# Kernel tuning notes

Hardware: AMD Instinct MI355X
Metric: run time of the kernel (lower is better)

Reference implementation:

```python
import jax, jax.numpy as jnp
import numpy as np

D_MODEL = 768
N_HEADS = 12
HEAD_DIM = D_MODEL // N_HEADS
D_FF = 4 * D_MODEL
EPS = 1e-5


def setup_inputs() -> dict:
    key = jax.random.key(0)
    ks = jax.random.split(key, 16)
    s = 0.02
    x = jax.random.normal(ks[0], (2, 2048, D_MODEL), dtype=jnp.float32)
    wq = jax.random.normal(ks[1], (D_MODEL, D_MODEL), dtype=jnp.float32) * s
    bq = jnp.zeros((D_MODEL,), jnp.float32)
    wk = jax.random.normal(ks[2], (D_MODEL, D_MODEL), dtype=jnp.float32) * s
    bk = jnp.zeros((D_MODEL,), jnp.float32)
    wv = jax.random.normal(ks[3], (D_MODEL, D_MODEL), dtype=jnp.float32) * s
    bv = jnp.zeros((D_MODEL,), jnp.float32)
    wo = jax.random.normal(ks[4], (D_MODEL, D_MODEL), dtype=jnp.float32) * s
    bo = jnp.zeros((D_MODEL,), jnp.float32)
    w1 = jax.random.normal(ks[5], (D_MODEL, D_FF), dtype=jnp.float32) * s
    b1 = jnp.zeros((D_FF,), jnp.float32)
    w2 = jax.random.normal(ks[6], (D_FF, D_MODEL), dtype=jnp.float32) * s
    b2 = jnp.zeros((D_MODEL,), jnp.float32)
    ln1_g = jnp.ones((D_MODEL,), jnp.float32)
    ln1_b = jnp.zeros((D_MODEL,), jnp.float32)
    ln2_g = jnp.ones((D_MODEL,), jnp.float32)
    ln2_b = jnp.zeros((D_MODEL,), jnp.float32)
    return dict(x=x, wq=wq, bq=bq, wk=wk, bk=bk, wv=wv, bv=bv, wo=wo, bo=bo,
                w1=w1, b1=b1, w2=w2, b2=b2,
                ln1_g=ln1_g, ln1_b=ln1_b, ln2_g=ln2_g, ln2_b=ln2_b)


def _layernorm(x, g, b):
    mu = jnp.mean(x, axis=-1, keepdims=True)
    var = jnp.mean(jnp.square(x - mu), axis=-1, keepdims=True)
    return (x - mu) * jax.lax.rsqrt(var + EPS) * g + b


def _attention(x, wq, bq, wk, bk, wv, bv, wo, bo):
    B, S, D = x.shape
    def split_heads(t):  # [B,S,D] -> [B,H,S,Hd]
        return t.reshape(B, S, N_HEADS, HEAD_DIM).transpose(0, 2, 1, 3)
    q = split_heads(x @ wq + bq)
    k = split_heads(x @ wk + bk)
    v = split_heads(x @ wv + bv)
    scores = jnp.einsum('bhqd,bhkd->bhqk', q, k) / np.sqrt(HEAD_DIM).astype(np.float32)
    causal = jnp.tril(jnp.ones((S, S), dtype=bool))
    scores = jnp.where(causal, scores, -jnp.inf)
    weights = jax.nn.softmax(scores, axis=-1)
    attn = jnp.einsum('bhqk,bhkd->bhqd', weights, v)
    attn = attn.transpose(0, 2, 1, 3).reshape(B, S, D)
    return attn @ wo + bo


def reference(x, wq, bq, wk, bk, wv, bv, wo, bo, w1, b1, w2, b2,
              ln1_g, ln1_b, ln2_g, ln2_b):
    x = x + _attention(_layernorm(x, ln1_g, ln1_b), wq, bq, wk, bk, wv, bv, wo, bo)
    h = _layernorm(x, ln2_g, ln2_b)
    ff = jax.nn.relu(h @ w1 + b1) @ w2 + b2
    return x + ff
```

## Files before the change

kernel.cpp:

```cpp
#include <hip/hip_runtime.h>
#include <stdint.h>

typedef __bf16 bf16;
typedef float f32x4 __attribute__((ext_vector_type(4)));
typedef bf16 bf16x8 __attribute__((ext_vector_type(8)));
typedef bf16 bf16x4 __attribute__((ext_vector_type(4)));

#define MFMA16(a, b, c) __builtin_amdgcn_mfma_f32_16x16x32_bf16((a), (b), (c), 0, 0, 0)

static __device__ __forceinline__ void load_lds16(const bf16* g, bf16* l) {
  __builtin_amdgcn_global_load_lds(
      (const __attribute__((address_space(1))) void*)g,
      (__attribute__((address_space(3))) void*)l, 16, 0, 0);
}

__global__ void __launch_bounds__(256) k_transpose(
    const float* s0, const float* s1, const float* s2, const float* s3,
    const float* s4, const float* s5,
    bf16* d0, bf16* d1, bf16* d2, bf16* d3, bf16* d4, bf16* d5) {
  int z = blockIdx.z;
  const float* src; bf16* dst; int R, C;
  switch (z) {
    case 0: src = s0; dst = d0; R = 768;  C = 768;  break;
    case 1: src = s1; dst = d1; R = 768;  C = 768;  break;
    case 2: src = s2; dst = d2; R = 768;  C = 768;  break;
    case 3: src = s3; dst = d3; R = 768;  C = 768;  break;
    case 4: src = s4; dst = d4; R = 768;  C = 3072; break;
    default: src = s5; dst = d5; R = 3072; C = 768; break;
  }
  int tcn = C >> 5;
  int nt = (R >> 5) * tcn;
  int t = blockIdx.x;
  if (t >= nt) return;
  int tr = t / tcn, tc = t % tcn;
  __shared__ float tile[32][33];
  int tx = threadIdx.x & 31, ty = threadIdx.x >> 5;
  for (int i = 0; i < 4; i++)
    tile[ty + i * 8][tx] = src[(size_t)(tr * 32 + ty + i * 8) * C + tc * 32 + tx];
  __syncthreads();
  for (int i = 0; i < 4; i++)
    dst[(size_t)(tc * 32 + ty + i * 8) * R + tr * 32 + tx] = (bf16)tile[tx][ty + i * 8];
}

__global__ void __launch_bounds__(256) k_layernorm(
    const float* __restrict__ in, const float* __restrict__ gam,
    const float* __restrict__ bet, bf16* __restrict__ out) {
  int row = blockIdx.x, tid = threadIdx.x;
  const float* rp = in + (size_t)row * 768;
  float v0 = rp[tid], v1 = rp[tid + 256], v2 = rp[tid + 512];
  float s = v0 + v1 + v2, sq = v0 * v0 + v1 * v1 + v2 * v2;
  for (int off = 1; off < 64; off <<= 1) {
    s += __shfl_xor(s, off, 64);
    sq += __shfl_xor(sq, off, 64);
  }
  __shared__ float ps[8];
  if ((tid & 63) == 0) { ps[tid >> 6] = s; ps[4 + (tid >> 6)] = sq; }
  __syncthreads();
  s = ps[0] + ps[1] + ps[2] + ps[3];
  sq = ps[4] + ps[5] + ps[6] + ps[7];
  float mu = s * (1.0f / 768.0f);
  float rstd = rsqrtf(sq * (1.0f / 768.0f) - mu * mu + 1e-5f);
  bf16* op = out + (size_t)row * 768;
  op[tid] = (bf16)((v0 - mu) * rstd * gam[tid] + bet[tid]);
  op[tid + 256] = (bf16)((v1 - mu) * rstd * gam[tid + 256] + bet[tid + 256]);
  op[tid + 512] = (bf16)((v2 - mu) * rstd * gam[tid + 512] + bet[tid + 512]);
}

__global__ void __launch_bounds__(256) k_ln2_reduce(
    const float* __restrict__ p0, const float* __restrict__ p1,
    const float* __restrict__ x, const float* __restrict__ bo,
    const float* __restrict__ gam, const float* __restrict__ bet,
    float* __restrict__ x1, bf16* __restrict__ h2) {
  int row = blockIdx.x, tid = threadIdx.x;
  size_t base = (size_t)row * 768;
  float v0 = p0[base + tid] + p1[base + tid] + x[base + tid] + bo[tid];
  float v1 = p0[base + tid + 256] + p1[base + tid + 256] + x[base + tid + 256] + bo[tid + 256];
  float v2 = p0[base + tid + 512] + p1[base + tid + 512] + x[base + tid + 512] + bo[tid + 512];
  x1[base + tid] = v0; x1[base + tid + 256] = v1; x1[base + tid + 512] = v2;
  float s = v0 + v1 + v2, sq = v0 * v0 + v1 * v1 + v2 * v2;
  for (int off = 1; off < 64; off <<= 1) {
    s += __shfl_xor(s, off, 64);
    sq += __shfl_xor(sq, off, 64);
  }
  __shared__ float ps[8];
  if ((tid & 63) == 0) { ps[tid >> 6] = s; ps[4 + (tid >> 6)] = sq; }
  __syncthreads();
  s = ps[0] + ps[1] + ps[2] + ps[3];
  sq = ps[4] + ps[5] + ps[6] + ps[7];
  float mu = s * (1.0f / 768.0f);
  float rstd = rsqrtf(sq * (1.0f / 768.0f) - mu * mu + 1e-5f);
  bf16* op = h2 + base;
  op[tid] = (bf16)((v0 - mu) * rstd * gam[tid] + bet[tid]);
  op[tid + 256] = (bf16)((v1 - mu) * rstd * gam[tid + 256] + bet[tid + 256]);
  op[tid + 512] = (bf16)((v2 - mu) * rstd * gam[tid + 512] + bet[tid + 512]);
}

__global__ void __launch_bounds__(256) k_ff2_reduce(
    const float* __restrict__ f0, const float* __restrict__ f1,
    const float* __restrict__ f2, const float* __restrict__ f3,
    const float* __restrict__ x1, const float* __restrict__ b2,
    float* __restrict__ out) {
  size_t i = ((size_t)blockIdx.x * 256 + threadIdx.x) * 4;
  int col = (int)(i % 768);
  f32x4 v = *(const f32x4*)(x1 + i);
  f32x4 b = *(const f32x4*)(b2 + col);
  f32x4 a0 = *(const f32x4*)(f0 + i), a1 = *(const f32x4*)(f1 + i);
  f32x4 a2 = *(const f32x4*)(f2 + i), a3 = *(const f32x4*)(f3 + i);
  *(f32x4*)(out + i) = v + b + a0 + a1 + a2 + a3;
}

template <int MT>
static __device__ __forceinline__ void gemm_core(
    const bf16* __restrict__ A, int lda, const bf16* __restrict__ Bt, int ldb,
    int Kc, int m0, int n0, bf16* As, bf16* Bs, f32x4 acc[MT][4]) {
  int tid = threadIdx.x, w = tid >> 6, lane = tid & 63, quad = lane >> 4, l15 = lane & 15;
  int wr = w >> 1, wc = w & 1;
  int srow = lane >> 2, sk = (lane & 3) * 8;
  for (int k0 = 0; k0 < Kc; k0 += 32) {
    __syncthreads();
    if (MT == 4) {
      for (int c = 0; c < 2; c++) {
        int seg = w * 2 + c;
        load_lds16(A + (size_t)(m0 + seg * 16 + srow) * lda + k0 + sk, As + seg * 512);
      }
    } else {
      load_lds16(A + (size_t)(m0 + w * 16 + srow) * lda + k0 + sk, As + w * 512);
    }
    for (int c = 0; c < 2; c++) {
      int seg = w * 2 + c;
      load_lds16(Bt + (size_t)(n0 + seg * 16 + srow) * ldb + k0 + sk, Bs + seg * 512);
    }
    __syncthreads();
    bf16x8 af[MT], bfr[4];
    for (int mi = 0; mi < MT; mi++)
      af[mi] = *(const bf16x8*)(As + (wr * (MT * 16) + mi * 16 + l15) * 32 + quad * 8);
    for (int ni = 0; ni < 4; ni++)
      bfr[ni] = *(const bf16x8*)(Bs + (wc * 64 + ni * 16 + l15) * 32 + quad * 8);
    for (int mi = 0; mi < MT; mi++)
      for (int ni = 0; ni < 4; ni++)
        acc[mi][ni] = MFMA16(af[mi], bfr[ni], acc[mi][ni]);
  }
}

template <int MT>
__global__ void __launch_bounds__(256) k_gemm(
    const bf16* __restrict__ A, const bf16* __restrict__ Bt,
    const float* __restrict__ bias, bf16* __restrict__ outp, int K_, int N_) {
  __shared__ __align__(16) bf16 As[MT * 32 * 32];
  __shared__ __align__(16) bf16 Bs[128 * 32];
  int m0 = blockIdx.y * (MT * 32), n0 = blockIdx.x * 128;
  f32x4 acc[MT][4] = {};
  gemm_core<MT>(A, K_, Bt, K_, K_, m0, n0, As, Bs, acc);
  int tid = threadIdx.x, w = tid >> 6, lane = tid & 63, quad = lane >> 4, l15 = lane & 15;
  int wr = w >> 1, wc = w & 1;
  float bv[4];
  for (int ni = 0; ni < 4; ni++) bv[ni] = bias[n0 + wc * 64 + ni * 16 + l15];
  for (int mi = 0; mi < MT; mi++) {
    int mb = m0 + wr * (MT * 16) + mi * 16 + quad * 4;
    for (int ni = 0; ni < 4; ni++) {
      int n = n0 + wc * 64 + ni * 16 + l15;
      for (int r = 0; r < 4; r++) {
        float val = acc[mi][ni][r] + bv[ni];
        outp[(size_t)(mb + r) * N_ + n] = (bf16)fmaxf(val, 0.0f);
      }
    }
  }
}

template <int MT>
__global__ void __launch_bounds__(256) k_gemm_split(
    const bf16* __restrict__ A, const bf16* __restrict__ Bt,
    float* __restrict__ f0, float* __restrict__ f1,
    float* __restrict__ f2, float* __restrict__ f3, int K_, int Kc, int N_) {
  __shared__ __align__(16) bf16 As[MT * 32 * 32];
  __shared__ __align__(16) bf16 Bs[128 * 32];
  int z = blockIdx.z;
  float* outp = (z == 0) ? f0 : (z == 1) ? f1 : (z == 2) ? f2 : f3;
  int m0 = blockIdx.y * (MT * 32), n0 = blockIdx.x * 128;
  f32x4 acc[MT][4] = {};
  gemm_core<MT>(A + (size_t)z * Kc, K_, Bt + (size_t)z * Kc, K_, Kc, m0, n0, As, Bs, acc);
  int tid = threadIdx.x, w = tid >> 6, lane = tid & 63, quad = lane >> 4, l15 = lane & 15;
  int wr = w >> 1, wc = w & 1;
  for (int mi = 0; mi < MT; mi++) {
    int mb = m0 + wr * (MT * 16) + mi * 16 + quad * 4;
    for (int ni = 0; ni < 4; ni++) {
      int n = n0 + wc * 64 + ni * 16 + l15;
      for (int r = 0; r < 4; r++)
        outp[(size_t)(mb + r) * N_ + n] = acc[mi][ni][r];
    }
  }
}

template <int MT>
__global__ void __launch_bounds__(256) k_gemm_qkv(
    const bf16* __restrict__ h1, const bf16* __restrict__ wqT,
    const bf16* __restrict__ wkT, const bf16* __restrict__ wvT,
    const float* __restrict__ bq, const float* __restrict__ bk,
    const float* __restrict__ bv, bf16* __restrict__ qb,
    bf16* __restrict__ kb, bf16* __restrict__ vtb) {
  __shared__ __align__(16) bf16 As[MT * 32 * 32];
  __shared__ __align__(16) bf16 Bs[128 * 32];
  int z = blockIdx.z;
  const bf16* Bt = (z == 0) ? wqT : (z == 1) ? wkT : wvT;
  const float* bias = (z == 0) ? bq : (z == 1) ? bk : bv;
  int m0 = blockIdx.y * (MT * 32), n0 = blockIdx.x * 128;
  f32x4 acc[MT][4] = {};
  gemm_core<MT>(h1, 768, Bt, 768, 768, m0, n0, As, Bs, acc);
  int tid = threadIdx.x, w = tid >> 6, lane = tid & 63, quad = lane >> 4, l15 = lane & 15;
  int wr = w >> 1, wc = w & 1;
  float bvv[4];
  for (int ni = 0; ni < 4; ni++) bvv[ni] = bias[n0 + wc * 64 + ni * 16 + l15];
  for (int mi = 0; mi < MT; mi++) {
    int mb = m0 + wr * (MT * 16) + mi * 16 + quad * 4;
    int b = mb >> 11, s0_ = mb & 2047;
    for (int ni = 0; ni < 4; ni++) {
      int n = n0 + wc * 64 + ni * 16 + l15;
      int h = n >> 6, hd = n & 63;
      if (z < 2) {
        bf16* outp = (z == 0) ? qb : kb;
        size_t base = (size_t)(b * 12 + h) * 2048 * 64;
        for (int r = 0; r < 4; r++)
          outp[base + (size_t)(s0_ + r) * 64 + hd] = (bf16)(acc[mi][ni][r] + bvv[ni]);
      } else {
        bf16x4 pk;
        for (int r = 0; r < 4; r++) pk[r] = (bf16)(acc[mi][ni][r] + bvv[ni]);
        *(bf16x4*)(vtb + (((size_t)(b * 12 + h) * 64 + hd) * 2048 + s0_)) = pk;
      }
    }
  }
}

__global__ void __launch_bounds__(256) k_attn(
    const bf16* __restrict__ qb, const bf16* __restrict__ kb,
    const bf16* __restrict__ vtb, bf16* __restrict__ out) {
  __shared__ __align__(16) bf16 Ks[128 * 64];
  __shared__ __align__(16) bf16 Vs[64 * 128];
  __shared__ __align__(16) bf16 Ps[4][16 * 128];
  int qt = 31 - (blockIdx.x / 24);
  int bh = blockIdx.x % 24;
  int q0 = qt * 64;
  int tid = threadIdx.x, w = tid >> 6, lane = tid & 63, quad = lane >> 4, l15 = lane & 15;
  const bf16* qbase = qb + (size_t)bh * 2048 * 64;
  const bf16* kbase = kb + (size_t)bh * 2048 * 64;
  const bf16* vbase = vtb + (size_t)bh * 64 * 2048;

  bf16x8 qf[2];
  for (int ds = 0; ds < 2; ds++)
    qf[ds] = *(const bf16x8*)(qbase + (size_t)(q0 + w * 16 + l15) * 64 + ds * 32 + quad * 8);

  f32x4 o[4] = {};
  f32x4 l_i = {};

  const float C2 = 0.18033688011112042f;
  int nkt = (qt >> 1) + 1;
  for (int kt = 0; kt < nkt; kt++) {
    int k0 = kt * 128;
    __syncthreads();
    {
      int rsub = lane >> 3, c8 = lane & 7;
      for (int c = 0; c < 4; c++) {
        int seg = c * 4 + w;
        int row = seg * 8 + rsub;
        load_lds16(kbase + (size_t)(k0 + row) * 64 + ((c8 ^ (row & 7)) * 8), Ks + seg * 512);
      }
      int rsub2 = lane >> 4, c16 = lane & 15;
      for (int c = 0; c < 4; c++) {
        int seg = c * 4 + w;
        int row = seg * 4 + rsub2;
        load_lds16(vbase + (size_t)row * 2048 + k0 + ((c16 ^ (row & 15)) * 8), Vs + seg * 512);
      }
    }
    __syncthreads();

    f32x4 sc[8] = {};
    for (int kj = 0; kj < 8; kj++) {
      int krow = kj * 16 + l15;
      for (int ds = 0; ds < 2; ds++) {
        bf16x8 kf = *(const bf16x8*)(Ks + krow * 64 + (((ds * 4 + quad) ^ (krow & 7)) * 8));
        sc[kj] = MFMA16(qf[ds], kf, sc[kj]);
      }
    }
    if (kt == nkt - 1) {
      int qg = q0 + w * 16 + quad * 4;
      for (int kj = 0; kj < 8; kj++) {
        int kg = k0 + kj * 16 + l15;
        for (int r = 0; r < 4; r++)
          if (kg > qg + r) sc[kj][r] = -3.0e38f;
      }
    }
    f32x4 lsum = {};
    for (int kj = 0; kj < 8; kj++)
      for (int r = 0; r < 4; r++) {
        float p = exp2f(sc[kj][r] * C2);
        sc[kj][r] = p;
        lsum[r] += p;
      }
    for (int off = 1; off < 16; off <<= 1)
      for (int r = 0; r < 4; r++) lsum[r] += __shfl_xor(lsum[r], off, 64);
    for (int r = 0; r < 4; r++) l_i[r] += lsum[r];
    for (int kj = 0; kj < 8; kj++) {
      int colb = kj * 16 + l15;
      int chb = colb >> 3, cin = colb & 7;
      for (int r = 0; r < 4; r++) {
        int prow = quad * 4 + r;
        Ps[w][prow * 128 + ((chb ^ prow) * 8) + cin] = (bf16)sc[kj][r];
      }
    }
    for (int ks = 0; ks < 4; ks++) {
      int prow = l15;
      bf16x8 pf = *(const bf16x8*)(&Ps[w][prow * 128 + (((ks * 4 + quad) ^ prow) * 8)]);
      for (int dj = 0; dj < 4; dj++) {
        int vrow = dj * 16 + l15;
        bf16x8 vf = *(const bf16x8*)(Vs + vrow * 128 + (((ks * 4 + quad) ^ (vrow & 15)) * 8));
        o[dj] = MFMA16(pf, vf, o[dj]);
      }
    }
  }
  int b = bh / 12, h = bh % 12;
  f32x4 rl;
  for (int r = 0; r < 4; r++) rl[r] = 1.0f / l_i[r];
  int srow = q0 + w * 16 + quad * 4;
  for (int dj = 0; dj < 4; dj++) {
    int d = h * 64 + dj * 16 + l15;
    for (int r = 0; r < 4; r++)
      out[(size_t)(b * 2048 + srow + r) * 768 + d] = (bf16)(o[dj][r] * rl[r]);
  }
}

extern "C" void kernel_launch(void* const* d_in, const int* in_sizes, int n_in,
                              void* d_out, int out_size, void* d_ws, size_t ws_size,
                              hipStream_t stream) {
  const float* x    = (const float*)d_in[0];
  const float* wq   = (const float*)d_in[1];
  const float* bq   = (const float*)d_in[2];
  const float* wk   = (const float*)d_in[3];
  const float* bk   = (const float*)d_in[4];
  const float* wv   = (const float*)d_in[5];
  const float* bv   = (const float*)d_in[6];
  const float* wo   = (const float*)d_in[7];
  const float* bo   = (const float*)d_in[8];
  const float* w1   = (const float*)d_in[9];
  const float* b1   = (const float*)d_in[10];
  const float* w2   = (const float*)d_in[11];
  const float* b2   = (const float*)d_in[12];
  const float* ln1g = (const float*)d_in[13];
  const float* ln1b = (const float*)d_in[14];
  const float* ln2g = (const float*)d_in[15];
  const float* ln2b = (const float*)d_in[16];

  char* p = (char*)d_ws;
  bf16* wqT = (bf16*)p; p += (size_t)768 * 768 * 2;
  bf16* wkT = (bf16*)p; p += (size_t)768 * 768 * 2;
  bf16* wvT = (bf16*)p; p += (size_t)768 * 768 * 2;
  bf16* woT = (bf16*)p; p += (size_t)768 * 768 * 2;
  bf16* w1T = (bf16*)p; p += (size_t)768 * 3072 * 2;
  bf16* w2T = (bf16*)p; p += (size_t)768 * 3072 * 2;
  bf16* h1   = (bf16*)p; p += (size_t)4096 * 768 * 2;
  bf16* qbuf = (bf16*)p; p += (size_t)4096 * 768 * 2;
  bf16* kbuf = (bf16*)p; p += (size_t)4096 * 768 * 2;
  bf16* vtb  = (bf16*)p; p += (size_t)4096 * 768 * 2;
  bf16* att  = (bf16*)p; p += (size_t)4096 * 768 * 2;
  float* x1  = (float*)p; p += (size_t)4096 * 768 * 4;
  bf16* h2   = (bf16*)p; p += (size_t)4096 * 768 * 2;
  bf16* ffm  = (bf16*)p; p += (size_t)4096 * 3072 * 2;
  float* p0  = (float*)p; p += (size_t)4096 * 768 * 4;
  float* p1  = (float*)p; p += (size_t)4096 * 768 * 4;
  float* f0 = (float*)h1;
  float* f1 = (float*)kbuf;
  float* f2 = p0;
  float* f3 = p1;

  k_transpose<<<dim3(2304, 1, 6), dim3(256), 0, stream>>>(
      wq, wk, wv, wo, w1, w2, wqT, wkT, wvT, woT, w1T, w2T);
  k_layernorm<<<dim3(4096), dim3(256), 0, stream>>>(x, ln1g, ln1b, h1);
  k_gemm_qkv<2><<<dim3(6, 64, 3), dim3(256), 0, stream>>>(
      h1, wqT, wkT, wvT, bq, bk, bv, qbuf, kbuf, vtb);
  k_attn<<<dim3(768), dim3(256), 0, stream>>>(qbuf, kbuf, vtb, att);
  k_gemm_split<2><<<dim3(6, 64, 2), dim3(256), 0, stream>>>(
      att, woT, p0, p1, p0, p1, 768, 384, 768);
  k_ln2_reduce<<<dim3(4096), dim3(256), 0, stream>>>(
      p0, p1, x, bo, ln2g, ln2b, x1, h2);
  k_gemm<2><<<dim3(24, 64), dim3(256), 0, stream>>>(
      h2, w1T, b1, ffm, 768, 3072);
  k_gemm_split<2><<<dim3(6, 64, 4), dim3(256), 0, stream>>>(
      ffm, w2T, f0, f1, f2, f3, 3072, 768, 768);
  k_ff2_reduce<<<dim3(3072), dim3(256), 0, stream>>>(
      f0, f1, f2, f3, x1, b2, (float*)d_out);
}
```

Baseline: 316.8 us.

## Replace split-K partial buffers with atomic accumulation and enlarge GEMM tiles

Split-K GEMMs now atomically add their partial sums straight into the residual buffers, which are pre-seeded with residual plus bias by the layernorm kernels. This removes the separate reduce kernels and the partial-buffer traffic. All GEMMs move to 128x128 tiles with a changed LDS load/read layout, so each block gets more reuse but the grids have fewer blocks. Float atomics make the summation order nondeterministic and add atomic traffic to global memory.

```diff
diff --git a/kernel.cpp b/kernel.cpp
--- a/kernel.cpp
+++ b/kernel.cpp
@@ -12,6 +12,10 @@
   __builtin_amdgcn_global_load_lds(
       (const __attribute__((address_space(1))) void*)g,
       (__attribute__((address_space(3))) void*)l, 16, 0, 0);
+}
+
+static __device__ __forceinline__ void atomAdd(float* p, float v) {
+  __hip_atomic_fetch_add(p, v, __ATOMIC_RELAXED, __HIP_MEMORY_SCOPE_AGENT);
 }
 
 __global__ void __launch_bounds__(256) k_transpose(
@@ -42,9 +46,10 @@
     dst[(size_t)(tc * 32 + ty + i * 8) * R + tr * 32 + tx] = (bf16)tile[tx][ty + i * 8];
 }
 
-__global__ void __launch_bounds__(256) k_layernorm(
+__global__ void __launch_bounds__(256) k_layernorm1(
     const float* __restrict__ in, const float* __restrict__ gam,
-    const float* __restrict__ bet, bf16* __restrict__ out) {
+    const float* __restrict__ bet, const float* __restrict__ bo,
+    bf16* __restrict__ out, float* __restrict__ x1init) {
   int row = blockIdx.x, tid = threadIdx.x;
   const float* rp = in + (size_t)row * 768;
   float v0 = rp[tid], v1 = rp[tid + 256], v2 = rp[tid + 512];
@@ -60,23 +65,23 @@
   sq = ps[4] + ps[5] + ps[6] + ps[7];
   float mu = s * (1.0f / 768.0f);
   float rstd = rsqrtf(sq * (1.0f / 768.0f) - mu * mu + 1e-5f);
-  bf16* op = out + (size_t)row * 768;
+  size_t base = (size_t)row * 768;
+  bf16* op = out + base;
   op[tid] = (bf16)((v0 - mu) * rstd * gam[tid] + bet[tid]);
   op[tid + 256] = (bf16)((v1 - mu) * rstd * gam[tid + 256] + bet[tid + 256]);
   op[tid + 512] = (bf16)((v2 - mu) * rstd * gam[tid + 512] + bet[tid + 512]);
-}
-
-__global__ void __launch_bounds__(256) k_ln2_reduce(
-    const float* __restrict__ p0, const float* __restrict__ p1,
-    const float* __restrict__ x, const float* __restrict__ bo,
-    const float* __restrict__ gam, const float* __restrict__ bet,
-    float* __restrict__ x1, bf16* __restrict__ h2) {
+  x1init[base + tid] = v0 + bo[tid];
+  x1init[base + tid + 256] = v1 + bo[tid + 256];
+  x1init[base + tid + 512] = v2 + bo[tid + 512];
+}
+
+__global__ void __launch_bounds__(256) k_layernorm2(
+    const float* __restrict__ x1, const float* __restrict__ gam,
+    const float* __restrict__ bet, const float* __restrict__ b2,
+    bf16* __restrict__ h2, float* __restrict__ dout) {
   int row = blockIdx.x, tid = threadIdx.x;
-  size_t base = (size_t)row * 768;
-  float v0 = p0[base + tid] + p1[base + tid] + x[base + tid] + bo[tid];
-  float v1 = p0[base + tid + 256] + p1[base + tid + 256] + x[base + tid + 256] + bo[tid + 256];
-  float v2 = p0[base + tid + 512] + p1[base + tid + 512] + x[base + tid + 512] + bo[tid + 512];
-  x1[base + tid] = v0; x1[base + tid + 256] = v1; x1[base + tid + 512] = v2;
+  const float* rp = x1 + (size_t)row * 768;
+  float v0 = rp[tid], v1 = rp[tid + 256], v2 = rp[tid + 512];
   float s = v0 + v1 + v2, sq = v0 * v0 + v1 * v1 + v2 * v2;
   for (int off = 1; off < 64; off <<= 1) {
     s += __shfl_xor(s, off, 64);
@@ -89,129 +94,104 @@
   sq = ps[4] + ps[5] + ps[6] + ps[7];
   float mu = s * (1.0f / 768.0f);
   float rstd = rsqrtf(sq * (1.0f / 768.0f) - mu * mu + 1e-5f);
+  size_t base = (size_t)row * 768;
   bf16* op = h2 + base;
   op[tid] = (bf16)((v0 - mu) * rstd * gam[tid] + bet[tid]);
   op[tid + 256] = (bf16)((v1 - mu) * rstd * gam[tid + 256] + bet[tid + 256]);
   op[tid + 512] = (bf16)((v2 - mu) * rstd * gam[tid + 512] + bet[tid + 512]);
-}
-
-__global__ void __launch_bounds__(256) k_ff2_reduce(
-    const float* __restrict__ f0, const float* __restrict__ f1,
-    const float* __restrict__ f2, const float* __restrict__ f3,
-    const float* __restrict__ x1, const float* __restrict__ b2,
-    float* __restrict__ out) {
-  size_t i = ((size_t)blockIdx.x * 256 + threadIdx.x) * 4;
-  int col = (int)(i % 768);
-  f32x4 v = *(const f32x4*)(x1 + i);
-  f32x4 b = *(const f32x4*)(b2 + col);
-  f32x4 a0 = *(const f32x4*)(f0 + i), a1 = *(const f32x4*)(f1 + i);
-  f32x4 a2 = *(const f32x4*)(f2 + i), a3 = *(const f32x4*)(f3 + i);
-  *(f32x4*)(out + i) = v + b + a0 + a1 + a2 + a3;
-}
-
-template <int MT>
+  dout[base + tid] = v0 + b2[tid];
+  dout[base + tid + 256] = v1 + b2[tid + 256];
+  dout[base + tid + 512] = v2 + b2[tid + 512];
+}
+
 static __device__ __forceinline__ void gemm_core(
     const bf16* __restrict__ A, int lda, const bf16* __restrict__ Bt, int ldb,
-    int Kc, int m0, int n0, bf16* As, bf16* Bs, f32x4 acc[MT][4]) {
+    int Kc, int m0, int n0, bf16* As, bf16* Bs, f32x4 acc[4][4]) {
   int tid = threadIdx.x, w = tid >> 6, lane = tid & 63, quad = lane >> 4, l15 = lane & 15;
   int wr = w >> 1, wc = w & 1;
-  int srow = lane >> 2, sk = (lane & 3) * 8;
+  int srow = lane & 15, sk = (lane >> 4) * 8;
   for (int k0 = 0; k0 < Kc; k0 += 32) {
     __syncthreads();
-    if (MT == 4) {
-      for (int c = 0; c < 2; c++) {
-        int seg = w * 2 + c;
-        load_lds16(A + (size_t)(m0 + seg * 16 + srow) * lda + k0 + sk, As + seg * 512);
-      }
-    } else {
-      load_lds16(A + (size_t)(m0 + w * 16 + srow) * lda + k0 + sk, As + w * 512);
-    }
     for (int c = 0; c < 2; c++) {
       int seg = w * 2 + c;
+      load_lds16(A + (size_t)(m0 + seg * 16 + srow) * lda + k0 + sk, As + seg * 512);
       load_lds16(Bt + (size_t)(n0 + seg * 16 + srow) * ldb + k0 + sk, Bs + seg * 512);
     }
     __syncthreads();
-    bf16x8 af[MT], bfr[4];
-    for (int mi = 0; mi < MT; mi++)
-      af[mi] = *(const bf16x8*)(As + (wr * (MT * 16) + mi * 16 + l15) * 32 + quad * 8);
+    bf16x8 af[4], bfr[4];
+    for (int mi = 0; mi < 4; mi++)
+      af[mi] = *(const bf16x8*)(As + (wr * 4 + mi) * 512 + quad * 128 + l15 * 8);
     for (int ni = 0; ni < 4; ni++)
-      bfr[ni] = *(const bf16x8*)(Bs + (wc * 64 + ni * 16 + l15) * 32 + quad * 8);
-    for (int mi = 0; mi < MT; mi++)
+      bfr[ni] = *(const bf16x8*)(Bs + (wc * 4 + ni) * 512 + quad * 128 + l15 * 8);
+    for (int mi = 0; mi < 4; mi++)
       for (int ni = 0; ni < 4; ni++)
         acc[mi][ni] = MFMA16(af[mi], bfr[ni], acc[mi][ni]);
   }
 }
 
-template <int MT>
-__global__ void __launch_bounds__(256) k_gemm(
+__global__ void __launch_bounds__(256) k_gemm_relu(
     const bf16* __restrict__ A, const bf16* __restrict__ Bt,
     const float* __restrict__ bias, bf16* __restrict__ outp, int K_, int N_) {
-  __shared__ __align__(16) bf16 As[MT * 32 * 32];
+  __shared__ __align__(16) bf16 As[128 * 32];
   __shared__ __align__(16) bf16 Bs[128 * 32];
-  int m0 = blockIdx.y * (MT * 32), n0 = blockIdx.x * 128;
-  f32x4 acc[MT][4] = {};
-  gemm_core<MT>(A, K_, Bt, K_, K_, m0, n0, As, Bs, acc);
+  int m0 = blockIdx.y * 128, n0 = blockIdx.x * 128;
+  f32x4 acc[4][4] = {};
+  gemm_core(A, K_, Bt, K_, K_, m0, n0, As, Bs, acc);
   int tid = threadIdx.x, w = tid >> 6, lane = tid & 63, quad = lane >> 4, l15 = lane & 15;
   int wr = w >> 1, wc = w & 1;
   float bv[4];
   for (int ni = 0; ni < 4; ni++) bv[ni] = bias[n0 + wc * 64 + ni * 16 + l15];
-  for (int mi = 0; mi < MT; mi++) {
-    int mb = m0 + wr * (MT * 16) + mi * 16 + quad * 4;
-    for (int ni = 0; ni < 4; ni++) {
-      int n = n0 + wc * 64 + ni * 16 + l15;
-      for (int r = 0; r < 4; r++) {
-        float val = acc[mi][ni][r] + bv[ni];
-        outp[(size_t)(mb + r) * N_ + n] = (bf16)fmaxf(val, 0.0f);
-      }
-    }
-  }
-}
-
-template <int MT>
-__global__ void __launch_bounds__(256) k_gemm_split(
-    const bf16* __restrict__ A, const bf16* __restrict__ Bt,
-    float* __restrict__ f0, float* __restrict__ f1,
-    float* __restrict__ f2, float* __restrict__ f3, int K_, int Kc, int N_) {
-  __shared__ __align__(16) bf16 As[MT * 32 * 32];
-  __shared__ __align__(16) bf16 Bs[128 * 32];
-  int z = blockIdx.z;
-  float* outp = (z == 0) ? f0 : (z == 1) ? f1 : (z == 2) ? f2 : f3;
-  int m0 = blockIdx.y * (MT * 32), n0 = blockIdx.x * 128;
-  f32x4 acc[MT][4] = {};
-  gemm_core<MT>(A + (size_t)z * Kc, K_, Bt + (size_t)z * Kc, K_, Kc, m0, n0, As, Bs, acc);
-  int tid = threadIdx.x, w = tid >> 6, lane = tid & 63, quad = lane >> 4, l15 = lane & 15;
-  int wr = w >> 1, wc = w & 1;
-  for (int mi = 0; mi < MT; mi++) {
-    int mb = m0 + wr * (MT * 16) + mi * 16 + quad * 4;
+  for (int mi = 0; mi < 4; mi++) {
+    int mb = m0 + wr * 64 + mi * 16 + quad * 4;
     for (int ni = 0; ni < 4; ni++) {
       int n = n0 + wc * 64 + ni * 16 + l15;
       for (int r = 0; r < 4; r++)
-        outp[(size_t)(mb + r) * N_ + n] = acc[mi][ni][r];
-    }
-  }
-}
-
-template <int MT>
+        outp[(size_t)(mb + r) * N_ + n] = (bf16)fmaxf(acc[mi][ni][r] + bv[ni], 0.0f);
+    }
+  }
+}
+
+__global__ void __launch_bounds__(256) k_gemm_split(
+    const bf16* __restrict__ A, const bf16* __restrict__ Bt,
+    float* __restrict__ outp, int K_, int Kc, int N_) {
+  __shared__ __align__(16) bf16 As[128 * 32];
+  __shared__ __align__(16) bf16 Bs[128 * 32];
+  int z = blockIdx.z;
+  int m0 = blockIdx.y * 128, n0 = blockIdx.x * 128;
+  f32x4 acc[4][4] = {};
+  gemm_core(A + (size_t)z * Kc, K_, Bt + (size_t)z * Kc, K_, Kc, m0, n0, As, Bs, acc);
+  int tid = threadIdx.x, w = tid >> 6, lane = tid & 63, quad = lane >> 4, l15 = lane & 15;
+  int wr = w >> 1, wc = w & 1;
+  for (int mi = 0; mi < 4; mi++) {
+    int mb = m0 + wr * 64 + mi * 16 + quad * 4;
+    for (int ni = 0; ni < 4; ni++) {
+      int n = n0 + wc * 64 + ni * 16 + l15;
+      for (int r = 0; r < 4; r++)
+        atomAdd(&outp[(size_t)(mb + r) * N_ + n], acc[mi][ni][r]);
+    }
+  }
+}
+
 __global__ void __launch_bounds__(256) k_gemm_qkv(
     const bf16* __restrict__ h1, const bf16* __restrict__ wqT,
     const bf16* __restrict__ wkT, const bf16* __restrict__ wvT,
     const float* __restrict__ bq, const float* __restrict__ bk,
     const float* __restrict__ bv, bf16* __restrict__ qb,
     bf16* __restrict__ kb, bf16* __restrict__ vtb) {
-  __shared__ __align__(16) bf16 As[MT * 32 * 32];
+  __shared__ __align__(16) bf16 As[128 * 32];
   __shared__ __align__(16) bf16 Bs[128 * 32];
   int z = blockIdx.z;
   const bf16* Bt = (z == 0) ? wqT : (z == 1) ? wkT : wvT;
   const float* bias = (z == 0) ? bq : (z == 1) ? bk : bv;
-  int m0 = blockIdx.y * (MT * 32), n0 = blockIdx.x * 128;
-  f32x4 acc[MT][4] = {};
-  gemm_core<MT>(h1, 768, Bt, 768, 768, m0, n0, As, Bs, acc);
+  int m0 = blockIdx.y * 128, n0 = blockIdx.x * 128;
+  f32x4 acc[4][4] = {};
+  gemm_core(h1, 768, Bt, 768, 768, m0, n0, As, Bs, acc);
   int tid = threadIdx.x, w = tid >> 6, lane = tid & 63, quad = lane >> 4, l15 = lane & 15;
   int wr = w >> 1, wc = w & 1;
   float bvv[4];
   for (int ni = 0; ni < 4; ni++) bvv[ni] = bias[n0 + wc * 64 + ni * 16 + l15];
-  for (int mi = 0; mi < MT; mi++) {
-    int mb = m0 + wr * (MT * 16) + mi * 16 + quad * 4;
+  for (int mi = 0; mi < 4; mi++) {
+    int mb = m0 + wr * 64 + mi * 16 + quad * 4;
     int b = mb >> 11, s0_ = mb & 2047;
     for (int ni = 0; ni < 4; ni++) {
       int n = n0 + wc * 64 + ni * 16 + l15;
@@ -363,27 +343,19 @@
   float* x1  = (float*)p; p += (size_t)4096 * 768 * 4;
   bf16* h2   = (bf16*)p; p += (size_t)4096 * 768 * 2;
   bf16* ffm  = (bf16*)p; p += (size_t)4096 * 3072 * 2;
-  float* p0  = (float*)p; p += (size_t)4096 * 768 * 4;
-  float* p1  = (float*)p; p += (size_t)4096 * 768 * 4;
-  float* f0 = (float*)h1;
-  float* f1 = (float*)kbuf;
-  float* f2 = p0;
-  float* f3 = p1;
 
   k_transpose<<<dim3(2304, 1, 6), dim3(256), 0, stream>>>(
       wq, wk, wv, wo, w1, w2, wqT, wkT, wvT, woT, w1T, w2T);
-  k_layernorm<<<dim3(4096), dim3(256), 0, stream>>>(x, ln1g, ln1b, h1);
-  k_gemm_qkv<2><<<dim3(6, 64, 3), dim3(256), 0, stream>>>(
+  k_layernorm1<<<dim3(4096), dim3(256), 0, stream>>>(x, ln1g, ln1b, bo, h1, x1);
+  k_gemm_qkv<<<dim3(6, 32, 3), dim3(256), 0, stream>>>(
       h1, wqT, wkT, wvT, bq, bk, bv, qbuf, kbuf, vtb);
   k_attn<<<dim3(768), dim3(256), 0, stream>>>(qbuf, kbuf, vtb, att);
-  k_gemm_split<2><<<dim3(6, 64, 2), dim3(256), 0, stream>>>(
-      att, woT, p0, p1, p0, p1, 768, 384, 768);
-  k_ln2_reduce<<<dim3(4096), dim3(256), 0, stream>>>(
-      p0, p1, x, bo, ln2g, ln2b, x1, h2);
-  k_gemm<2><<<dim3(24, 64), dim3(256), 0, stream>>>(
+  k_gemm_split<<<dim3(6, 32, 4), dim3(256), 0, stream>>>(
+      att, woT, x1, 768, 192, 768);
+  k_layernorm2<<<dim3(4096), dim3(256), 0, stream>>>(
+      x1, ln2g, ln2b, b2, h2, (float*)d_out);
+  k_gemm_relu<<<dim3(24, 32), dim3(256), 0, stream>>>(
       h2, w1T, b1, ffm, 768, 3072);
-  k_gemm_split<2><<<dim3(6, 64, 4), dim3(256), 0, stream>>>(
-      ffm, w2T, f0, f1, f2, f3, 3072, 768, 768);
-  k_ff2_reduce<<<dim3(3072), dim3(256), 0, stream>>>(
-      f0, f1, f2, f3, x1, b2, (float*)d_out);
-}
+  k_gemm_split<<<dim3(6, 32, 4), dim3(256), 0, stream>>>(
+      ffm, w2T, (float*)d_out, 3072, 768, 768);
+}
```

Result: slower. 365.5 us (+15.4%).
